# Kernel tuning notes

Hardware: AMD Instinct MI355X
Metric: run time of the kernel (lower is better)

The kernel has to match this reference:

```python
import jax, jax.numpy as jnp
import numpy as np

G, N, F_IN, H, C = 128, 512, 128, 128, 10
LAMB = 1.0
NEG_SLOPE = 0.2
P_EDGE = 32.0 / N  # avg degree ~32


def setup_inputs() -> dict:
    key = jax.random.key(0)
    ks = jax.random.split(key, 12)
    x = jax.random.normal(ks[0], (G, N, F_IN), dtype=jnp.float32)
    # symmetric 0/1 adjacency without self loops (per-graph dense block)
    a = (jax.random.uniform(ks[1], (G, N, N)) < P_EDGE).astype(jnp.float32)
    adj = jnp.maximum(a, jnp.swapaxes(a, 1, 2)) * (1.0 - jnp.eye(N, dtype=jnp.float32))

    def lin(k, fi, fo):
        return (jax.random.normal(k, (fi, fo), dtype=jnp.float32) / np.float32(np.sqrt(fi)))

    return {
        "x": x, "adj": adj,
        "W1": lin(ks[2], F_IN, H), "b1": jnp.zeros((H,), jnp.float32),
        "W2": lin(ks[3], H, H), "b2": jnp.zeros((H,), jnp.float32),
        "W3": lin(ks[4], H, H), "b3": jnp.zeros((H,), jnp.float32),
        "att1_s": 0.1 * jax.random.normal(ks[5], (H,), dtype=jnp.float32),
        "att1_d": 0.1 * jax.random.normal(ks[6], (H,), dtype=jnp.float32),
        "att2_s": 0.1 * jax.random.normal(ks[7], (H,), dtype=jnp.float32),
        "att2_d": 0.1 * jax.random.normal(ks[8], (H,), dtype=jnp.float32),
        "Wl1": lin(ks[9], 2 * H, H), "bl1": jnp.zeros((H,), jnp.float32),
        "Wl2": lin(ks[10], H, H // 2), "bl2": jnp.zeros((H // 2,), jnp.float32),
        "Wl3": lin(ks[11], H // 2, C), "bl3": jnp.zeros((C,), jnp.float32),
    }


def gcn(x, adj, W, b):
    # GCNConv: D^{-1/2} (A + I) D^{-1/2} X W + b  (self-loop weight 1, edge weights in adj)
    deg = adj.sum(-1) + 1.0                              # [G, n]
    dinv = jax.lax.rsqrt(deg)
    xw = x @ W                                           # [G, n, H]
    agg = jnp.einsum('gij,gjf->gif', adj, dinv[..., None] * xw)
    return dinv[..., None] * agg + (dinv * dinv)[..., None] * xw + b


def info_score(x, adj):
    # HGP-SL node information score: row-wise L1 norm of (I - D^{-1} A) X
    deg = jnp.maximum(adj.sum(-1), 1.0)
    agg = jnp.einsum('gij,gjf->gif', adj, x) / deg[..., None]
    return jnp.sum(jnp.abs(x - agg), axis=-1)            # [G, n]


def hgpsl_pool(x, adj, att_s, att_d, k):
    # top-k node selection by information score, then structure learning:
    # dense (sample=False) path: e_ij = leaky_relu(att.[x_i||x_j]) + lamb*A_ij, softmax over j
    s = info_score(x, adj)
    _, idx = jax.lax.top_k(s, k)                         # [G, k]
    xk = jnp.take_along_axis(x, idx[..., None], axis=1)  # [G, k, H]
    g = jnp.arange(x.shape[0])[:, None, None]
    ak = adj[g, idx[:, :, None], idx[:, None, :]]        # induced adjacency [G, k, k]
    e = jax.nn.leaky_relu((xk @ att_s)[:, :, None] + (xk @ att_d)[:, None, :], NEG_SLOPE)
    attn = jax.nn.softmax(e + LAMB * ak, axis=-1)        # new learned edge weights
    return xk, attn


def readout(x):
    # gmp || gap over nodes
    return jnp.concatenate([x.max(axis=1), x.mean(axis=1)], axis=-1)


def reference(x, adj, W1, b1, W2, b2, W3, b3, att1_s, att1_d, att2_s, att2_d,
              Wl1, bl1, Wl2, bl2, Wl3, bl3):
    h = jax.nn.relu(gcn(x, adj, W1, b1))
    h, a1 = hgpsl_pool(h, adj, att1_s, att1_d, N // 2)
    x1 = readout(h)
    h = jax.nn.relu(gcn(h, a1, W2, b2))
    h, a2 = hgpsl_pool(h, a1, att2_s, att2_d, N // 4)
    x2 = readout(h)
    h = jax.nn.relu(gcn(h, a2, W3, b3))
    x3 = readout(h)
    z = jax.nn.relu(x1) + jax.nn.relu(x2) + jax.nn.relu(x3)
    z = jax.nn.relu(z @ Wl1 + bl1)
    z = jax.nn.relu(z @ Wl2 + bl2)
    return jax.nn.softmax(z @ Wl3 + bl3, axis=-1)
```

## Files before the change

### kernel.cpp

```cpp
#include <hip/hip_runtime.h>

#define Gg   128
#define N1   512
#define FH   128
#define K1   256
#define K2   128

typedef unsigned short ush;
typedef __bf16 bf16x8 __attribute__((ext_vector_type(8)));
typedef float  floatx4 __attribute__((ext_vector_type(4)));

__device__ inline float wredsum(float v) {
#pragma unroll
    for (int o = 32; o; o >>= 1) v += __shfl_xor(v, o, 64);
    return v;
}
__device__ inline float wredmax(float v) {
#pragma unroll
    for (int o = 32; o; o >>= 1) v = fmaxf(v, __shfl_xor(v, o, 64));
    return v;
}
__device__ inline ush bf_rne(float x) {
    unsigned u = __float_as_uint(x);
    return (ush)((u + 0x7fffu + ((u >> 16) & 1u)) >> 16);
}
__device__ inline float bf2f(ush u) { return __uint_as_float((unsigned)u << 16); }
__device__ inline void split3(float v, ush& h, ush& m, ush& l) {
    h = bf_rne(v);
    float r1 = v - bf2f(h);
    m = bf_rne(r1);
    l = bf_rne(r1 - bf2f(m));
}

__global__ __launch_bounds__(256) void k_prep(const float* __restrict__ adj,
        float* __restrict__ dinv_gcn, float* __restrict__ dinv_info,
        unsigned* __restrict__ adjbits) {
    int wave = threadIdx.x >> 6, lane = threadIdx.x & 63;
    long long row = (long long)blockIdx.x * 4 + wave;
    const float* ar = adj + row * N1;
    float s = 0.f;
    unsigned myw = 0;
#pragma unroll
    for (int c = 0; c < 8; ++c) {
        float v = ar[c * 64 + lane];
        s += v;
        unsigned long long mk = __ballot(v != 0.0f);
        unsigned lo = (unsigned)mk, hi = (unsigned)(mk >> 32);
        if ((lane >> 1) == c) myw = (lane & 1) ? hi : lo;
    }
    if (lane < 16) adjbits[row * 16 + lane] = myw;
    s = wredsum(s);
    if (lane == 0) {
        dinv_gcn[row]  = rsqrtf(s + 1.0f);
        dinv_info[row] = 1.0f / fmaxf(s, 1.0f);
    }
}

__global__ __launch_bounds__(256) void k_gemm_rw(const float* __restrict__ A,
        const float* __restrict__ W, float* __restrict__ C,
        const float* __restrict__ rs) {
    __shared__ float Al[64][68];
    __shared__ float Wl[64][132];
    long long row0 = (long long)blockIdx.x * 64;
    int tid = threadIdx.x, tr = tid >> 4, tc = tid & 15;
    float acc[4][8] = {};
    for (int ch = 0; ch < 2; ++ch) {
        for (int p = tid; p < 1024; p += 256) {
            int r = p >> 4, c4 = p & 15;
            *(float4*)&Al[r][c4 * 4] = *(const float4*)(A + (row0 + r) * 128 + ch * 64 + c4 * 4);
        }
        for (int p = tid; p < 2048; p += 256) {
            int r = p >> 5, c4 = p & 31;
            *(float4*)&Wl[r][c4 * 4] = *(const float4*)(W + (ch * 64 + r) * 128 + c4 * 4);
        }
        __syncthreads();
        for (int k = 0; k < 64; ++k) {
            float4 w0 = *(const float4*)&Wl[k][tc * 8];
            float4 w1 = *(const float4*)&Wl[k][tc * 8 + 4];
            float w[8] = {w0.x, w0.y, w0.z, w0.w, w1.x, w1.y, w1.z, w1.w};
#pragma unroll
            for (int i = 0; i < 4; ++i) {
                float a = Al[tr * 4 + i][k];
#pragma unroll
                for (int j = 0; j < 8; ++j) acc[i][j] = fmaf(a, w[j], acc[i][j]);
            }
        }
        __syncthreads();
    }
#pragma unroll
    for (int i = 0; i < 4; ++i) {
        long long r = row0 + tr * 4 + i;
        float sc = rs ? rs[r] : 1.0f;
        *(float4*)(C + r * 128 + tc * 8)     = make_float4(sc * acc[i][0], sc * acc[i][1], sc * acc[i][2], sc * acc[i][3]);
        *(float4*)(C + r * 128 + tc * 8 + 4) = make_float4(sc * acc[i][4], sc * acc[i][5], sc * acc[i][6], sc * acc[i][7]);
    }
}

__global__ __launch_bounds__(256) void k_tsplit(const float* __restrict__ feat,
        ush* __restrict__ Thi, ush* __restrict__ Tmid, ush* __restrict__ Tlo) {
    __shared__ float tile[64 * 65];
    int b = blockIdx.x;
    int g = b >> 4, rb = (b >> 1) & 7, cb = b & 1;
    int t = threadIdx.x;
    {
        int r0 = t >> 4, c4 = t & 15;
#pragma unroll
        for (int i = 0; i < 4; ++i) {
            int r = r0 + i * 16;
            float4 v = *(const float4*)(feat + ((long long)g * 512 + rb * 64 + r) * 128 + cb * 64 + c4 * 4);
            tile[r * 65 + c4 * 4 + 0] = v.x;
            tile[r * 65 + c4 * 4 + 1] = v.y;
            tile[r * 65 + c4 * 4 + 2] = v.z;
            tile[r * 65 + c4 * 4 + 3] = v.w;
        }
    }
    __syncthreads();
    int tf = t >> 2, chunk = t & 3;
    ush hbuf[16] __attribute__((aligned(16)));
    ush mbuf[16] __attribute__((aligned(16)));
    ush lbuf[16] __attribute__((aligned(16)));
#pragma unroll
    for (int i = 0; i < 16; ++i) {
        int m = chunk * 16 + i;
        split3(tile[m * 65 + tf], hbuf[i], mbuf[i], lbuf[i]);
    }
    long long obase = ((long long)g * 128 + cb * 64 + tf) * 512 + rb * 64 + chunk * 16;
    *(uint4*)(Thi + obase)      = *(const uint4*)&hbuf[0];
    *(uint4*)(Thi + obase + 8)  = *(const uint4*)&hbuf[8];
    *(uint4*)(Tmid + obase)     = *(const uint4*)&mbuf[0];
    *(uint4*)(Tmid + obase + 8) = *(const uint4*)&mbuf[8];
    *(uint4*)(Tlo + obase)      = *(const uint4*)&lbuf[0];
    *(uint4*)(Tlo + obase + 8)  = *(const uint4*)&lbuf[8];
}

template<int EPI>
__global__ __launch_bounds__(256) void k_aggb(const unsigned* __restrict__ adjbits,
        const ush* __restrict__ Bhi, const ush* __restrict__ Bmid, const ush* __restrict__ Blo,
        const float* __restrict__ dvec, const float* __restrict__ hx,
        const float* __restrict__ bias, float* __restrict__ outH, float* __restrict__ outS) {
    __shared__ unsigned bitsL[64 * 17];
    __shared__ float sred[2][64];
    int b = blockIdx.x;
    int g  = (b & 7) + ((b >> 6) << 3);
    int rb = (b >> 3) & 7;
    int tid = threadIdx.x;
    int w = tid >> 6, lane = tid & 63;
    int wm = w >> 1, wn = w & 1;
    int ln = lane & 15, quad = lane >> 4;
    {
        int r = tid >> 2, w4 = (tid & 3) * 4;
        uint4 v = *(const uint4*)(adjbits + ((long long)(g * 512 + rb * 64 + r)) * 16 + w4);
        bitsL[r * 17 + w4 + 0] = v.x; bitsL[r * 17 + w4 + 1] = v.y;
        bitsL[r * 17 + w4 + 2] = v.z; bitsL[r * 17 + w4 + 3] = v.w;
    }
    __syncthreads();
    floatx4 acc[2][4];
#pragma unroll
    for (int i = 0; i < 2; ++i)
#pragma unroll
        for (int j = 0; j < 4; ++j) { floatx4 z = {0.f, 0.f, 0.f, 0.f}; acc[i][j] = z; }

    const long long bb = (long long)g * 128 * 512;
    for (int kt = 0; kt < 16; ++kt) {
        int kk = kt * 32;
        bf16x8 af[2];
#pragma unroll
        for (int tm = 0; tm < 2; ++tm) {
            unsigned word = bitsL[(wm * 32 + tm * 16 + ln) * 17 + kt];
            unsigned byte = (word >> (quad * 8)) & 0xffu;
            unsigned au[4] __attribute__((aligned(16)));
            au[0] = ((byte >> 0) & 1 ? 0x3F80u : 0u) | ((byte >> 1) & 1 ? 0x3F800000u : 0u);
            au[1] = ((byte >> 2) & 1 ? 0x3F80u : 0u) | ((byte >> 3) & 1 ? 0x3F800000u : 0u);
            au[2] = ((byte >> 4) & 1 ? 0x3F80u : 0u) | ((byte >> 5) & 1 ? 0x3F800000u : 0u);
            au[3] = ((byte >> 6) & 1 ? 0x3F80u : 0u) | ((byte >> 7) & 1 ? 0x3F800000u : 0u);
            af[tm] = *(const bf16x8*)au;
        }
#pragma unroll
        for (int tn = 0; tn < 4; ++tn) {
            long long off = bb + (long long)(wn * 64 + tn * 16 + ln) * 512 + kk + quad * 8;
            bf16x8 bh = *(const bf16x8*)(Bhi + off);
            bf16x8 bm = *(const bf16x8*)(Bmid + off);
            bf16x8 bl = *(const bf16x8*)(Blo + off);
#pragma unroll
            for (int tm = 0; tm < 2; ++tm) {
                acc[tm][tn] = __builtin_amdgcn_mfma_f32_16x16x32_bf16(af[tm], bh, acc[tm][tn], 0, 0, 0);
                acc[tm][tn] = __builtin_amdgcn_mfma_f32_16x16x32_bf16(af[tm], bm, acc[tm][tn], 0, 0, 0);
                acc[tm][tn] = __builtin_amdgcn_mfma_f32_16x16x32_bf16(af[tm], bl, acc[tm][tn], 0, 0, 0);
            }
        }
    }
    long long rowbase = (long long)g * 512 + rb * 64;
    if (EPI == 0) {
#pragma unroll
        for (int tm = 0; tm < 2; ++tm)
#pragma unroll
        for (int r = 0; r < 4; ++r) {
            long long grow = rowbase + wm * 32 + tm * 16 + quad * 4 + r;
            float di = dvec[grow];
#pragma unroll
            for (int tn = 0; tn < 4; ++tn) {
                int nc = wn * 64 + tn * 16 + ln;
                outH[grow * 128 + nc] =
                    fmaxf(fmaf(di, acc[tm][tn][r] + hx[grow * 128 + nc], bias[nc]), 0.f);
            }
        }
    } else {
#pragma unroll
        for (int tm = 0; tm < 2; ++tm)
#pragma unroll
        for (int r = 0; r < 4; ++r) {
            int ml = wm * 32 + tm * 16 + quad * 4 + r;
            long long grow = rowbase + ml;
            float di = dvec[grow];
            float v = 0.f;
#pragma unroll
            for (int tn = 0; tn < 4; ++tn) {
                int nc = wn * 64 + tn * 16 + ln;
                v += fabsf(hx[grow * 128 + nc] - acc[tm][tn][r] * di);
            }
            v += __shfl_xor(v, 1); v += __shfl_xor(v, 2);
            v += __shfl_xor(v, 4); v += __shfl_xor(v, 8);
            if (ln == 0) sred[wn][ml] = v;
        }
        __syncthreads();
        if (tid < 64) outS[rowbase + tid] = sred[0][tid] + sred[1][tid];
    }
}

template<int NT, int KSEL>
__global__ __launch_bounds__(256) void k_topk(const float* __restrict__ s, int* __restrict__ idx) {
    __shared__ unsigned long long keys[NT];
    int g = blockIdx.x;
    const float* sg = s + g * NT;
    for (int t = threadIdx.x; t < NT; t += 256) {
        unsigned int b = __float_as_uint(sg[t]);
        unsigned int ord = (b & 0x80000000u) ? ~b : (b | 0x80000000u);
        keys[t] = ((unsigned long long)(~ord) << 32) | (unsigned int)t;
    }
    __syncthreads();
    for (int k = 2; k <= NT; k <<= 1) {
        for (int j = k >> 1; j > 0; j >>= 1) {
            for (int i = threadIdx.x; i < NT; i += 256) {
                int l = i ^ j;
                if (l > i) {
                    bool dir = ((i & k) == 0);
                    unsigned long long a = keys[i], b2 = keys[l];
                    bool sw = dir ? (a > b2) : (a < b2);
                    if (sw) { keys[i] = b2; keys[l] = a; }
                }
            }
            __syncthreads();
        }
    }
    for (int t = threadIdx.x; t < KSEL; t += 256)
        idx[g * KSEL + t] = (int)(keys[t] & 0xffffffffu);
}

template<int KK>
__global__ __launch_bounds__(256) void k_gather(const float* __restrict__ h, int srcN,
        const int* __restrict__ idx, const float* __restrict__ atts, const float* __restrict__ attd,
        float* __restrict__ xk, float* __restrict__ as_, float* __restrict__ ad_) {
    int wave = threadIdx.x >> 6, lane = threadIdx.x & 63;
    int r = blockIdx.x * 4 + wave;
    int g = r / KK;
    int j = idx[r];
    float2 v = *(const float2*)(h + ((long long)g * srcN + j) * 128 + lane * 2);
    *(float2*)(xk + (long long)r * 128 + lane * 2) = v;
    float2 sv = *(const float2*)(atts + lane * 2);
    float2 dv = *(const float2*)(attd + lane * 2);
    float ps = v.x * sv.x + v.y * sv.y;
    float pd = v.x * dv.x + v.y * dv.y;
    ps = wredsum(ps); pd = wredsum(pd);
    if (lane == 0) { as_[r] = ps; ad_[r] = pd; }
}

__global__ __launch_bounds__(256) void k_attn1b(const unsigned* __restrict__ adjbits,
        const int* __restrict__ idx, const float* __restrict__ as_, const float* __restrict__ ad_,
        float* __restrict__ a1, float* __restrict__ dgo, float* __restrict__ dio) {
    __shared__ int   idxL[K1];
    __shared__ float adL[K1];
    __shared__ unsigned bitsW[4][20];
    int g = blockIdx.x / (K1 / 4);
    int wave = threadIdx.x >> 6, lane = threadIdx.x & 63;
    int i = (blockIdx.x % (K1 / 4)) * 4 + wave;
    for (int t = threadIdx.x; t < K1; t += 256) { idxL[t] = idx[g * K1 + t]; adL[t] = ad_[g * K1 + t]; }
    __syncthreads();
    int ri = idxL[i];
    if (lane < 4) {
        uint4 v = *(const uint4*)(adjbits + ((long long)(g * 512 + ri)) * 16 + lane * 4);
        bitsW[wave][lane * 4 + 0] = v.x; bitsW[wave][lane * 4 + 1] = v.y;
        bitsW[wave][lane * 4 + 2] = v.z; bitsW[wave][lane * 4 + 3] = v.w;
    }
    __syncthreads();
    float asi = as_[g * K1 + i];
    float vals[4];
    float m = -1e30f;
#pragma unroll
    for (int e = 0; e < 4; ++e) {
        int j = e * 64 + lane;
        float x = asi + adL[j];
        x = (x >= 0.f) ? x : 0.2f * x;
        int jj = idxL[j];
        unsigned bit = (bitsW[wave][jj >> 5] >> (jj & 31)) & 1u;
        x += (float)bit;
        vals[e] = x; m = fmaxf(m, x);
    }
    m = wredmax(m);
    float S = 0.f;
#pragma unroll
    for (int e = 0; e < 4; ++e) { vals[e] = expf(vals[e] - m); S += vals[e]; }
    S = wredsum(S);
    float inv = 1.f / S, rs = 0.f;
    float* orow = a1 + ((long long)g * K1 + i) * K1;
#pragma unroll
    for (int e = 0; e < 4; ++e) { float p = vals[e] * inv; rs += p; orow[e * 64 + lane] = p; }
    rs = wredsum(rs);
    if (lane == 0) { dgo[g * K1 + i] = rsqrtf(rs + 1.f); dio[g * K1 + i] = 1.f / fmaxf(rs, 1.f); }
}

template<int KK, int SRCN>
__global__ __launch_bounds__(256) void k_attn(const float* __restrict__ adjSrc,
        const int* __restrict__ idx, const float* __restrict__ as_, const float* __restrict__ ad_,
        float* __restrict__ attn, float* __restrict__ dgo, float* __restrict__ dio) {
    constexpr int E = KK / 64;
    __shared__ int   idxL[KK];
    __shared__ float adL[KK];
    __shared__ float rowL[4][SRCN];
    int bpg = KK / 4;
    int g = blockIdx.x / bpg;
    int wave = threadIdx.x >> 6, lane = threadIdx.x & 63;
    int i = (blockIdx.x % bpg) * 4 + wave;
    for (int t = threadIdx.x; t < KK; t += 256) { idxL[t] = idx[g * KK + t]; adL[t] = ad_[g * KK + t]; }
    __syncthreads();
    int ri = idxL[i];
    const float* arow = adjSrc + ((long long)g * SRCN + ri) * SRCN;
    for (int c = lane; c < SRCN; c += 64) rowL[wave][c] = arow[c];
    float asi = as_[g * KK + i];
    float vals[E];
    float m = -1e30f;
#pragma unroll
    for (int e = 0; e < E; ++e) {
        int j = e * 64 + lane;
        float x = asi + adL[j];
        x = (x >= 0.f) ? x : 0.2f * x;
        x += rowL[wave][idxL[j]];
        vals[e] = x; m = fmaxf(m, x);
    }
    m = wredmax(m);
    float S = 0.f;
#pragma unroll
    for (int e = 0; e < E; ++e) { vals[e] = expf(vals[e] - m); S += vals[e]; }
    S = wredsum(S);
    float inv = 1.f / S, rs = 0.f;
    float* orow = attn + ((long long)g * KK + i) * KK;
#pragma unroll
    for (int e = 0; e < E; ++e) { float p = vals[e] * inv; rs += p; orow[e * 64 + lane] = p; }
    rs = wredsum(rs);
    if (lane == 0) { dgo[g * KK + i] = rsqrtf(rs + 1.f); dio[g * KK + i] = 1.f / fmaxf(rs, 1.f); }
}

template<int KK>
__global__ __launch_bounds__(128) void k_readout(const float* __restrict__ xk, float* __restrict__ xo) {
    int g = blockIdx.x, f = threadIdx.x;
    const float* p = xk + (long long)g * KK * 128 + f;
    float m = -1e30f, s = 0.f;
    for (int r = 0; r < KK; ++r) { float v = p[r * 128]; m = fmaxf(m, v); s += v; }
    xo[g * 256 + f] = m;
    xo[g * 256 + 128 + f] = s * (1.0f / KK);
}

template<int KK, bool SCALEY, int EPI>
__global__ __launch_bounds__(256) void k_agg(const float* __restrict__ A, const float* __restrict__ Y,
        const float* __restrict__ dg, const float* __restrict__ di_,
        const float* __restrict__ bias, const float* __restrict__ hx,
        float* __restrict__ outH, float* __restrict__ outS) {
    __shared__ float Al[64][68];
    __shared__ float Yl[64][132];
    __shared__ float red[64][17];
    constexpr int RB = KK / 64;
    int g = blockIdx.x / RB;
    int rb = blockIdx.x % RB;
    const float* Ag = A + (long long)g * KK * KK;
    const float* Yg = Y + (long long)g * KK * 128;
    int tid = threadIdx.x, tr = tid >> 4, tc = tid & 15;
    float acc[4][8] = {};
    for (int ch = 0; ch < KK / 64; ++ch) {
        for (int p = tid; p < 1024; p += 256) {
            int r = p >> 4, c4 = p & 15;
            *(float4*)&Al[r][c4 * 4] = *(const float4*)(Ag + (rb * 64 + r) * KK + ch * 64 + c4 * 4);
        }
        for (int p = tid; p < 2048; p += 256) {
            int r = p >> 5, c4 = p & 31;
            float4 v = *(const float4*)(Yg + (ch * 64 + r) * 128 + c4 * 4);
            if (SCALEY) { float sc = dg[g * KK + ch * 64 + r]; v.x *= sc; v.y *= sc; v.z *= sc; v.w *= sc; }
            *(float4*)&Yl[r][c4 * 4] = v;
        }
        __syncthreads();
        for (int k = 0; k < 64; ++k) {
            float4 w0 = *(const float4*)&Yl[k][tc * 8];
            float4 w1 = *(const float4*)&Yl[k][tc * 8 + 4];
            float w[8] = {w0.x, w0.y, w0.z, w0.w, w1.x, w1.y, w1.z, w1.w};
#pragma unroll
            for (int i = 0; i < 4; ++i) {
                float a = Al[tr * 4 + i][k];
#pragma unroll
                for (int j = 0; j < 8; ++j) acc[i][j] = fmaf(a, w[j], acc[i][j]);
            }
        }
        __syncthreads();
    }
    int i0 = rb * 64 + tr * 4;
    if (EPI == 0) {
#pragma unroll
        for (int i = 0; i < 4; ++i) {
            long long gi = (long long)g * KK + i0 + i;
            float d = dg[gi], dd = d * d;
            float4 x0 = *(const float4*)(hx + gi * 128 + tc * 8);
            float4 x1 = *(const float4*)(hx + gi * 128 + tc * 8 + 4);
            float4 b0 = *(const float4*)(bias + tc * 8);
            float4 b1 = *(const float4*)(bias + tc * 8 + 4);
            float4 o0, o1;
            o0.x = fmaxf(fmaf(d, acc[i][0], fmaf(dd, x0.x, b0.x)), 0.f);
            o0.y = fmaxf(fmaf(d, acc[i][1], fmaf(dd, x0.y, b0.y)), 0.f);
            o0.z = fmaxf(fmaf(d, acc[i][2], fmaf(dd, x0.z, b0.z)), 0.f);
            o0.w = fmaxf(fmaf(d, acc[i][3], fmaf(dd, x0.w, b0.w)), 0.f);
            o1.x = fmaxf(fmaf(d, acc[i][4], fmaf(dd, x1.x, b1.x)), 0.f);
            o1.y = fmaxf(fmaf(d, acc[i][5], fmaf(dd, x1.y, b1.y)), 0.f);
            o1.z = fmaxf(fmaf(d, acc[i][6], fmaf(dd, x1.z, b1.z)), 0.f);
            o1.w = fmaxf(fmaf(d, acc[i][7], fmaf(dd, x1.w, b1.w)), 0.f);
            *(float4*)(outH + gi * 128 + tc * 8)     = o0;
            *(float4*)(outH + gi * 128 + tc * 8 + 4) = o1;
        }
    } else {
#pragma unroll
        for (int i = 0; i < 4; ++i) {
            long long gi = (long long)g * KK + i0 + i;
            float d = di_[gi];
            float4 x0 = *(const float4*)(hx + gi * 128 + tc * 8);
            float4 x1 = *(const float4*)(hx + gi * 128 + tc * 8 + 4);
            float p = fabsf(x0.x - acc[i][0] * d) + fabsf(x0.y - acc[i][1] * d)
                    + fabsf(x0.z - acc[i][2] * d) + fabsf(x0.w - acc[i][3] * d)
                    + fabsf(x1.x - acc[i][4] * d) + fabsf(x1.y - acc[i][5] * d)
                    + fabsf(x1.z - acc[i][6] * d) + fabsf(x1.w - acc[i][7] * d);
            red[tr * 4 + i][tc] = p;
        }
        __syncthreads();
        if (tid < 64) {
            float s = 0.f;
#pragma unroll
            for (int t = 0; t < 16; ++t) s += red[tid][t];
            outS[(long long)g * KK + rb * 64 + tid] = s;
        }
    }
}

__global__ __launch_bounds__(128) void k_mlp(const float* __restrict__ x1, const float* __restrict__ x2,
        const float* __restrict__ x3,
        const float* __restrict__ Wl1, const float* __restrict__ bl1,
        const float* __restrict__ Wl2, const float* __restrict__ bl2,
        const float* __restrict__ Wl3, const float* __restrict__ bl3,
        float* __restrict__ out) {
    __shared__ float z[256], z1[128], z2[64], lg[10];
    int g = blockIdx.x, t = threadIdx.x;
    for (int k = t; k < 256; k += 128)
        z[k] = fmaxf(x1[g * 256 + k], 0.f) + fmaxf(x2[g * 256 + k], 0.f) + fmaxf(x3[g * 256 + k], 0.f);
    __syncthreads();
    {
        float acc = bl1[t];
        for (int k = 0; k < 256; ++k) acc = fmaf(z[k], Wl1[k * 128 + t], acc);
        z1[t] = fmaxf(acc, 0.f);
    }
    __syncthreads();
    if (t < 64) {
        float acc = bl2[t];
        for (int k = 0; k < 128; ++k) acc = fmaf(z1[k], Wl2[k * 64 + t], acc);
        z2[t] = fmaxf(acc, 0.f);
    }
    __syncthreads();
    if (t < 10) {
        float acc = bl3[t];
        for (int k = 0; k < 64; ++k) acc = fmaf(z2[k], Wl3[k * 10 + t], acc);
        lg[t] = acc;
    }
    __syncthreads();
    if (t == 0) {
        float m = -1e30f;
        for (int c = 0; c < 10; ++c) m = fmaxf(m, lg[c]);
        float S = 0.f;
        float e[10];
        for (int c = 0; c < 10; ++c) { e[c] = expf(lg[c] - m); S += e[c]; }
        float inv = 1.f / S;
        for (int c = 0; c < 10; ++c) out[g * 10 + c] = e[c] * inv;
    }
}

extern "C" void kernel_launch(void* const* d_in, const int* in_sizes, int n_in,
                              void* d_out, int out_size, void* d_ws, size_t ws_size,
                              hipStream_t stream) {
    const float* x     = (const float*)d_in[0];
    const float* adj   = (const float*)d_in[1];
    const float* W1    = (const float*)d_in[2];
    const float* b1    = (const float*)d_in[3];
    const float* W2    = (const float*)d_in[4];
    const float* b2    = (const float*)d_in[5];
    const float* W3    = (const float*)d_in[6];
    const float* b3    = (const float*)d_in[7];
    const float* att1s = (const float*)d_in[8];
    const float* att1d = (const float*)d_in[9];
    const float* att2s = (const float*)d_in[10];
    const float* att2d = (const float*)d_in[11];
    const float* Wl1   = (const float*)d_in[12];
    const float* bl1   = (const float*)d_in[13];
    const float* Wl2   = (const float*)d_in[14];
    const float* bl2   = (const float*)d_in[15];
    const float* Wl3   = (const float*)d_in[16];
    const float* bl3   = (const float*)d_in[17];
    float* out = (float*)d_out;

    char* ws = (char*)d_ws;
    unsigned* adjbits = (unsigned*)(ws + 0);
    ush*   T1hi   = (ush*)  (ws + 8388608);
    ush*   T1mid  = (ush*)  (ws + 25165824);
    ush*   T1lo   = (ush*)  (ws + 41943040);
    ush*   T2hi   = (ush*)  (ws + 58720256);
    ush*   T2mid  = (ush*)  (ws + 75497472);
    ush*   T2lo   = (ush*)  (ws + 92274688);
    float* dxw1   = (float*)(ws + 109051904);
    float* h1     = dxw1;
    float* a1     = (float*)(ws + 142606336);
    float* xk1    = (float*)(ws + 176160768);
    float* xw2    = (float*)(ws + 192937984);
    float* h2     = (float*)(ws + 209715200);
    float* xk2    = (float*)(ws + 226492416);
    float* a2     = (float*)(ws + 234881024);
    float* xw3    = (float*)(ws + 243269632);
    float* h3     = (float*)(ws + 251658240);
    float* s1     = (float*)(ws + 260046848);
    int*   idx1   = (int*)  (ws + 260308992);
    float* as1    = (float*)(ws + 260571136);
    float* ad1    = (float*)(ws + 260702208);
    float* dinv_g1= (float*)(ws + 260833280);
    float* dinv_i1= (float*)(ws + 261095424);
    float* dinv_g2= (float*)(ws + 261357568);
    float* dinv_i2= (float*)(ws + 261488640);
    float* x1r    = (float*)(ws + 261619712);
    float* s2     = (float*)(ws + 261750784);
    int*   idx2   = (int*)  (ws + 261881856);
    float* as2    = (float*)(ws + 261947392);
    float* ad2    = (float*)(ws + 262012928);
    float* dinv_g3= (float*)(ws + 262078464);
    float* dinv_i3= (float*)(ws + 262144000);
    float* x2r    = (float*)(ws + 262209536);
    float* x3r    = (float*)(ws + 262340608);

    k_prep<<<Gg * N1 / 4, 256, 0, stream>>>(adj, dinv_g1, dinv_i1, adjbits);
    k_gemm_rw<<<Gg * N1 / 64, 256, 0, stream>>>(x, W1, dxw1, dinv_g1);
    k_tsplit<<<Gg * 16, 256, 0, stream>>>(dxw1, T1hi, T1mid, T1lo);
    k_aggb<0><<<Gg * 8, 256, 0, stream>>>(adjbits, T1hi, T1mid, T1lo, dinv_g1, dxw1, b1, h1, nullptr);
    k_tsplit<<<Gg * 16, 256, 0, stream>>>(h1, T2hi, T2mid, T2lo);
    k_aggb<1><<<Gg * 8, 256, 0, stream>>>(adjbits, T2hi, T2mid, T2lo, dinv_i1, h1, nullptr, nullptr, s1);
    k_topk<N1, K1><<<Gg, 256, 0, stream>>>(s1, idx1);
    k_gather<K1><<<Gg * K1 / 4, 256, 0, stream>>>(h1, N1, idx1, att1s, att1d, xk1, as1, ad1);
    k_readout<K1><<<Gg, 128, 0, stream>>>(xk1, x1r);
    k_attn1b<<<Gg * K1 / 4, 256, 0, stream>>>(adjbits, idx1, as1, ad1, a1, dinv_g2, dinv_i2);

    k_gemm_rw<<<Gg * K1 / 64, 256, 0, stream>>>(xk1, W2, xw2, nullptr);
    k_agg<K1, true, 0><<<Gg * (K1 / 64), 256, 0, stream>>>(a1, xw2, dinv_g2, dinv_i2, b2, xw2, h2, nullptr);
    k_agg<K1, false, 1><<<Gg * (K1 / 64), 256, 0, stream>>>(a1, h2, dinv_g2, dinv_i2, b2, h2, nullptr, s2);
    k_topk<K1, K2><<<Gg, 256, 0, stream>>>(s2, idx2);
    k_gather<K2><<<Gg * K2 / 4, 256, 0, stream>>>(h2, K1, idx2, att2s, att2d, xk2, as2, ad2);
    k_readout<K2><<<Gg, 128, 0, stream>>>(xk2, x2r);
    k_attn<K2, K1><<<Gg * K2 / 4, 256, 0, stream>>>(a1, idx2, as2, ad2, a2, dinv_g3, dinv_i3);

    k_gemm_rw<<<Gg * K2 / 64, 256, 0, stream>>>(xk2, W3, xw3, nullptr);
    k_agg<K2, true, 0><<<Gg * (K2 / 64), 256, 0, stream>>>(a2, xw3, dinv_g3, dinv_i3, b3, xw3, h3, nullptr);
    k_readout<K2><<<Gg, 128, 0, stream>>>(h3, x3r);

    k_mlp<<<Gg, 128, 0, stream>>>(x1r, x2r, x3r, Wl1, bl1, Wl2, bl2, Wl3, bl3, out);
}
```

Baseline: 708.1 us.

## Run pooled-graph aggregations on MFMA with 3-way bf16 split and prefetched loads

Replaces the fp32 FMA shared-memory aggregation kernels for the second and third GCN layers with MFMA-based kernels. Attention matrices and features are split into hi/mid/lo bf16 parts so products keep near-fp32 accuracy (six MFMA terms per tile). The attention kernels now write the split bf16 arrays directly, and the dense fp32 second attention matrix is no longer written. Adds register double-buffering of the B-operand loads in the layer-1 bitmask aggregation. This costs extra split kernels, a larger workspace and more MFMA work per output.

```diff
diff --git a/kernel.cpp b/kernel.cpp
--- a/kernel.cpp
+++ b/kernel.cpp
@@ -30,6 +30,15 @@
     float r1 = v - bf2f(h);
     m = bf_rne(r1);
     l = bf_rne(r1 - bf2f(m));
+}
+__device__ __forceinline__ bf16x8 expand_bits(unsigned word, int quad) {
+    unsigned byte = (word >> (quad * 8)) & 0xffu;
+    unsigned au[4] __attribute__((aligned(16)));
+    au[0] = ((byte & 1u)   ? 0x3F80u : 0u) | ((byte & 2u)   ? 0x3F800000u : 0u);
+    au[1] = ((byte & 4u)   ? 0x3F80u : 0u) | ((byte & 8u)   ? 0x3F800000u : 0u);
+    au[2] = ((byte & 16u)  ? 0x3F80u : 0u) | ((byte & 32u)  ? 0x3F800000u : 0u);
+    au[3] = ((byte & 64u)  ? 0x3F80u : 0u) | ((byte & 128u) ? 0x3F800000u : 0u);
+    return *(const bf16x8*)au;
 }
 
 __global__ __launch_bounds__(256) void k_prep(const float* __restrict__ adj,
@@ -96,18 +105,22 @@
     }
 }
 
+template<int KD>
 __global__ __launch_bounds__(256) void k_tsplit(const float* __restrict__ feat,
         ush* __restrict__ Thi, ush* __restrict__ Tmid, ush* __restrict__ Tlo) {
     __shared__ float tile[64 * 65];
     int b = blockIdx.x;
-    int g = b >> 4, rb = (b >> 1) & 7, cb = b & 1;
+    int cb = b & 1;
+    long long row0 = (long long)(b >> 1) * 64;
+    int g = (int)(row0 / KD);
+    int rk0 = (int)(row0 % KD);
     int t = threadIdx.x;
     {
         int r0 = t >> 4, c4 = t & 15;
 #pragma unroll
         for (int i = 0; i < 4; ++i) {
             int r = r0 + i * 16;
-            float4 v = *(const float4*)(feat + ((long long)g * 512 + rb * 64 + r) * 128 + cb * 64 + c4 * 4);
+            float4 v = *(const float4*)(feat + (row0 + r) * 128 + cb * 64 + c4 * 4);
             tile[r * 65 + c4 * 4 + 0] = v.x;
             tile[r * 65 + c4 * 4 + 1] = v.y;
             tile[r * 65 + c4 * 4 + 2] = v.z;
@@ -124,13 +137,64 @@
         int m = chunk * 16 + i;
         split3(tile[m * 65 + tf], hbuf[i], mbuf[i], lbuf[i]);
     }
-    long long obase = ((long long)g * 128 + cb * 64 + tf) * 512 + rb * 64 + chunk * 16;
+    long long obase = ((long long)g * 128 + cb * 64 + tf) * KD + rk0 + chunk * 16;
     *(uint4*)(Thi + obase)      = *(const uint4*)&hbuf[0];
     *(uint4*)(Thi + obase + 8)  = *(const uint4*)&hbuf[8];
     *(uint4*)(Tmid + obase)     = *(const uint4*)&mbuf[0];
     *(uint4*)(Tmid + obase + 8) = *(const uint4*)&mbuf[8];
     *(uint4*)(Tlo + obase)      = *(const uint4*)&lbuf[0];
     *(uint4*)(Tlo + obase + 8)  = *(const uint4*)&lbuf[8];
+}
+
+__device__ __forceinline__ void loadB4(const ush* __restrict__ Bhi, const ush* __restrict__ Bmid,
+        const ush* __restrict__ Blo, const long long* boff, int kk,
+        bf16x8* h, bf16x8* m, bf16x8* l) {
+#pragma unroll
+    for (int tn = 0; tn < 4; ++tn) {
+        h[tn] = *(const bf16x8*)(Bhi  + boff[tn] + kk);
+        m[tn] = *(const bf16x8*)(Bmid + boff[tn] + kk);
+        l[tn] = *(const bf16x8*)(Blo  + boff[tn] + kk);
+    }
+}
+__device__ __forceinline__ void loadA2(const ush* __restrict__ Ahi, const ush* __restrict__ Amid,
+        const ush* __restrict__ Alo, const long long* aoff, int kk,
+        bf16x8* h, bf16x8* m, bf16x8* l) {
+#pragma unroll
+    for (int tm = 0; tm < 2; ++tm) {
+        h[tm] = *(const bf16x8*)(Ahi  + aoff[tm] + kk);
+        m[tm] = *(const bf16x8*)(Amid + aoff[tm] + kk);
+        l[tm] = *(const bf16x8*)(Alo  + aoff[tm] + kk);
+    }
+}
+__device__ __forceinline__ void aggb_step(const unsigned* bitsL, int a0r, int a1r, int kt, int quad,
+        const bf16x8* Bh, const bf16x8* Bm, const bf16x8* Bl, floatx4 acc[2][4]) {
+    bf16x8 af0 = expand_bits(bitsL[a0r + kt], quad);
+    bf16x8 af1 = expand_bits(bitsL[a1r + kt], quad);
+#pragma unroll
+    for (int tn = 0; tn < 4; ++tn) {
+        acc[0][tn] = __builtin_amdgcn_mfma_f32_16x16x32_bf16(af0, Bh[tn], acc[0][tn], 0, 0, 0);
+        acc[1][tn] = __builtin_amdgcn_mfma_f32_16x16x32_bf16(af1, Bh[tn], acc[1][tn], 0, 0, 0);
+        acc[0][tn] = __builtin_amdgcn_mfma_f32_16x16x32_bf16(af0, Bm[tn], acc[0][tn], 0, 0, 0);
+        acc[1][tn] = __builtin_amdgcn_mfma_f32_16x16x32_bf16(af1, Bm[tn], acc[1][tn], 0, 0, 0);
+        acc[0][tn] = __builtin_amdgcn_mfma_f32_16x16x32_bf16(af0, Bl[tn], acc[0][tn], 0, 0, 0);
+        acc[1][tn] = __builtin_amdgcn_mfma_f32_16x16x32_bf16(af1, Bl[tn], acc[1][tn], 0, 0, 0);
+    }
+}
+__device__ __forceinline__ void aggs_step(const bf16x8* Ah, const bf16x8* Am, const bf16x8* Al,
+        const bf16x8* Bh, const bf16x8* Bm, const bf16x8* Bl, floatx4 acc[2][4]) {
+#pragma unroll
+    for (int tm = 0; tm < 2; ++tm)
+#pragma unroll
+    for (int tn = 0; tn < 4; ++tn) {
+        floatx4 a = acc[tm][tn];
+        a = __builtin_amdgcn_mfma_f32_16x16x32_bf16(Ah[tm], Bh[tn], a, 0, 0, 0);
+        a = __builtin_amdgcn_mfma_f32_16x16x32_bf16(Ah[tm], Bm[tn], a, 0, 0, 0);
+        a = __builtin_amdgcn_mfma_f32_16x16x32_bf16(Am[tm], Bh[tn], a, 0, 0, 0);
+        a = __builtin_amdgcn_mfma_f32_16x16x32_bf16(Ah[tm], Bl[tn], a, 0, 0, 0);
+        a = __builtin_amdgcn_mfma_f32_16x16x32_bf16(Al[tm], Bh[tn], a, 0, 0, 0);
+        a = __builtin_amdgcn_mfma_f32_16x16x32_bf16(Am[tm], Bm[tn], a, 0, 0, 0);
+        acc[tm][tn] = a;
+    }
 }
 
 template<int EPI>
@@ -161,35 +225,104 @@
         for (int j = 0; j < 4; ++j) { floatx4 z = {0.f, 0.f, 0.f, 0.f}; acc[i][j] = z; }
 
     const long long bb = (long long)g * 128 * 512;
-    for (int kt = 0; kt < 16; ++kt) {
-        int kk = kt * 32;
-        bf16x8 af[2];
-#pragma unroll
-        for (int tm = 0; tm < 2; ++tm) {
-            unsigned word = bitsL[(wm * 32 + tm * 16 + ln) * 17 + kt];
-            unsigned byte = (word >> (quad * 8)) & 0xffu;
-            unsigned au[4] __attribute__((aligned(16)));
-            au[0] = ((byte >> 0) & 1 ? 0x3F80u : 0u) | ((byte >> 1) & 1 ? 0x3F800000u : 0u);
-            au[1] = ((byte >> 2) & 1 ? 0x3F80u : 0u) | ((byte >> 3) & 1 ? 0x3F800000u : 0u);
-            au[2] = ((byte >> 4) & 1 ? 0x3F80u : 0u) | ((byte >> 5) & 1 ? 0x3F800000u : 0u);
-            au[3] = ((byte >> 6) & 1 ? 0x3F80u : 0u) | ((byte >> 7) & 1 ? 0x3F800000u : 0u);
-            af[tm] = *(const bf16x8*)au;
-        }
-#pragma unroll
-        for (int tn = 0; tn < 4; ++tn) {
-            long long off = bb + (long long)(wn * 64 + tn * 16 + ln) * 512 + kk + quad * 8;
-            bf16x8 bh = *(const bf16x8*)(Bhi + off);
-            bf16x8 bm = *(const bf16x8*)(Bmid + off);
-            bf16x8 bl = *(const bf16x8*)(Blo + off);
-#pragma unroll
-            for (int tm = 0; tm < 2; ++tm) {
-                acc[tm][tn] = __builtin_amdgcn_mfma_f32_16x16x32_bf16(af[tm], bh, acc[tm][tn], 0, 0, 0);
-                acc[tm][tn] = __builtin_amdgcn_mfma_f32_16x16x32_bf16(af[tm], bm, acc[tm][tn], 0, 0, 0);
-                acc[tm][tn] = __builtin_amdgcn_mfma_f32_16x16x32_bf16(af[tm], bl, acc[tm][tn], 0, 0, 0);
+    long long boff[4];
+#pragma unroll
+    for (int tn = 0; tn < 4; ++tn)
+        boff[tn] = bb + (long long)(wn * 64 + tn * 16 + ln) * 512 + quad * 8;
+    int a0r = (wm * 32 + ln) * 17;
+    int a1r = (wm * 32 + 16 + ln) * 17;
+
+    bf16x8 Xh[4], Xm[4], Xl[4], Yh[4], Ym[4], Yl[4];
+    loadB4(Bhi, Bmid, Blo, boff, 0, Xh, Xm, Xl);
+    for (int kt = 0; kt < 16; kt += 2) {
+        loadB4(Bhi, Bmid, Blo, boff, (kt + 1) * 32, Yh, Ym, Yl);
+        aggb_step(bitsL, a0r, a1r, kt, quad, Xh, Xm, Xl, acc);
+        if (kt + 2 < 16) loadB4(Bhi, Bmid, Blo, boff, (kt + 2) * 32, Xh, Xm, Xl);
+        aggb_step(bitsL, a0r, a1r, kt + 1, quad, Yh, Ym, Yl, acc);
+    }
+    long long rowbase = (long long)g * 512 + rb * 64;
+    if (EPI == 0) {
+#pragma unroll
+        for (int tm = 0; tm < 2; ++tm)
+#pragma unroll
+        for (int r = 0; r < 4; ++r) {
+            long long grow = rowbase + wm * 32 + tm * 16 + quad * 4 + r;
+            float di = dvec[grow];
+#pragma unroll
+            for (int tn = 0; tn < 4; ++tn) {
+                int nc = wn * 64 + tn * 16 + ln;
+                outH[grow * 128 + nc] =
+                    fmaxf(fmaf(di, acc[tm][tn][r] + hx[grow * 128 + nc], bias[nc]), 0.f);
             }
         }
-    }
-    long long rowbase = (long long)g * 512 + rb * 64;
+    } else {
+#pragma unroll
+        for (int tm = 0; tm < 2; ++tm)
+#pragma unroll
+        for (int r = 0; r < 4; ++r) {
+            int ml = wm * 32 + tm * 16 + quad * 4 + r;
+            long long grow = rowbase + ml;
+            float di = dvec[grow];
+            float v = 0.f;
+#pragma unroll
+            for (int tn = 0; tn < 4; ++tn) {
+                int nc = wn * 64 + tn * 16 + ln;
+                v += fabsf(hx[grow * 128 + nc] - acc[tm][tn][r] * di);
+            }
+            v += __shfl_xor(v, 1); v += __shfl_xor(v, 2);
+            v += __shfl_xor(v, 4); v += __shfl_xor(v, 8);
+            if (ln == 0) sred[wn][ml] = v;
+        }
+        __syncthreads();
+        if (tid < 64) outS[rowbase + tid] = sred[0][tid] + sred[1][tid];
+    }
+}
+
+template<int KD, int EPI>
+__global__ __launch_bounds__(256) void k_aggs(
+        const ush* __restrict__ Ahi, const ush* __restrict__ Amid, const ush* __restrict__ Alo,
+        const ush* __restrict__ Yhi, const ush* __restrict__ Ymid, const ush* __restrict__ Ylo,
+        const float* __restrict__ dvec, const float* __restrict__ hx,
+        const float* __restrict__ bias, float* __restrict__ outH, float* __restrict__ outS) {
+    __shared__ float sred[2][64];
+    constexpr int BPG = KD / 64;
+    constexpr int KT = KD / 32;
+    int b = blockIdx.x;
+    int g  = (b & 7) + ((b / (8 * BPG)) << 3);
+    int rb = (b >> 3) & (BPG - 1);
+    int tid = threadIdx.x;
+    int w = tid >> 6, lane = tid & 63;
+    int wm = w >> 1, wn = w & 1;
+    int ln = lane & 15, quad = lane >> 4;
+    floatx4 acc[2][4];
+#pragma unroll
+    for (int i = 0; i < 2; ++i)
+#pragma unroll
+        for (int j = 0; j < 4; ++j) { floatx4 z = {0.f, 0.f, 0.f, 0.f}; acc[i][j] = z; }
+
+    long long aoff[2], boff[4];
+#pragma unroll
+    for (int tm = 0; tm < 2; ++tm)
+        aoff[tm] = ((long long)g * KD + rb * 64 + wm * 32 + tm * 16 + ln) * KD + quad * 8;
+#pragma unroll
+    for (int tn = 0; tn < 4; ++tn)
+        boff[tn] = ((long long)g * 128 + wn * 64 + tn * 16 + ln) * KD + quad * 8;
+
+    bf16x8 XAh[2], XAm[2], XAl[2], YAh[2], YAm[2], YAl[2];
+    bf16x8 XBh[4], XBm[4], XBl[4], YBh[4], YBm[4], YBl[4];
+    loadA2(Ahi, Amid, Alo, aoff, 0, XAh, XAm, XAl);
+    loadB4(Yhi, Ymid, Ylo, boff, 0, XBh, XBm, XBl);
+    for (int kt = 0; kt < KT; kt += 2) {
+        loadA2(Ahi, Amid, Alo, aoff, (kt + 1) * 32, YAh, YAm, YAl);
+        loadB4(Yhi, Ymid, Ylo, boff, (kt + 1) * 32, YBh, YBm, YBl);
+        aggs_step(XAh, XAm, XAl, XBh, XBm, XBl, acc);
+        if (kt + 2 < KT) {
+            loadA2(Ahi, Amid, Alo, aoff, (kt + 2) * 32, XAh, XAm, XAl);
+            loadB4(Yhi, Ymid, Ylo, boff, (kt + 2) * 32, XBh, XBm, XBl);
+        }
+        aggs_step(YAh, YAm, YAl, YBh, YBm, YBl, acc);
+    }
+    long long rowbase = (long long)g * KD + rb * 64;
     if (EPI == 0) {
 #pragma unroll
         for (int tm = 0; tm < 2; ++tm)
@@ -276,10 +409,12 @@
 
 __global__ __launch_bounds__(256) void k_attn1b(const unsigned* __restrict__ adjbits,
         const int* __restrict__ idx, const float* __restrict__ as_, const float* __restrict__ ad_,
-        float* __restrict__ a1, float* __restrict__ dgo, float* __restrict__ dio) {
+        float* __restrict__ a1, ush* __restrict__ Ahi, ush* __restrict__ Amid, ush* __restrict__ Alo,
+        float* __restrict__ dgo, float* __restrict__ dio) {
     __shared__ int   idxL[K1];
     __shared__ float adL[K1];
     __shared__ unsigned bitsW[4][20];
+    __shared__ float rowL[4][K1];
     int g = blockIdx.x / (K1 / 4);
     int wave = threadIdx.x >> 6, lane = threadIdx.x & 63;
     int i = (blockIdx.x % (K1 / 4)) * 4 + wave;
@@ -313,33 +448,42 @@
     float inv = 1.f / S, rs = 0.f;
     float* orow = a1 + ((long long)g * K1 + i) * K1;
 #pragma unroll
-    for (int e = 0; e < 4; ++e) { float p = vals[e] * inv; rs += p; orow[e * 64 + lane] = p; }
+    for (int e = 0; e < 4; ++e) {
+        float p = vals[e] * inv; rs += p;
+        orow[e * 64 + lane] = p;
+        rowL[wave][e * 64 + lane] = p;
+    }
     rs = wredsum(rs);
     if (lane == 0) { dgo[g * K1 + i] = rsqrtf(rs + 1.f); dio[g * K1 + i] = 1.f / fmaxf(rs, 1.f); }
-}
-
-template<int KK, int SRCN>
-__global__ __launch_bounds__(256) void k_attn(const float* __restrict__ adjSrc,
+    long long sb = ((long long)g * K1 + i) * K1 + lane * 4;
+    ush hb[4], mb[4], lb[4];
+#pragma unroll
+    for (int q = 0; q < 4; ++q) split3(rowL[wave][lane * 4 + q], hb[q], mb[q], lb[q]);
+    *(ushort4*)(Ahi  + sb) = make_ushort4(hb[0], hb[1], hb[2], hb[3]);
+    *(ushort4*)(Amid + sb) = make_ushort4(mb[0], mb[1], mb[2], mb[3]);
+    *(ushort4*)(Alo  + sb) = make_ushort4(lb[0], lb[1], lb[2], lb[3]);
+}
+
+__global__ __launch_bounds__(256) void k_attn2(const float* __restrict__ a1,
         const int* __restrict__ idx, const float* __restrict__ as_, const float* __restrict__ ad_,
-        float* __restrict__ attn, float* __restrict__ dgo, float* __restrict__ dio) {
-    constexpr int E = KK / 64;
-    __shared__ int   idxL[KK];
-    __shared__ float adL[KK];
-    __shared__ float rowL[4][SRCN];
-    int bpg = KK / 4;
-    int g = blockIdx.x / bpg;
+        ush* __restrict__ Ahi, ush* __restrict__ Amid, ush* __restrict__ Alo,
+        float* __restrict__ dgo) {
+    __shared__ int   idxL[K2];
+    __shared__ float adL[K2];
+    __shared__ float rowL[4][K1];
+    int g = blockIdx.x / (K2 / 4);
     int wave = threadIdx.x >> 6, lane = threadIdx.x & 63;
-    int i = (blockIdx.x % bpg) * 4 + wave;
-    for (int t = threadIdx.x; t < KK; t += 256) { idxL[t] = idx[g * KK + t]; adL[t] = ad_[g * KK + t]; }
+    int i = (blockIdx.x % (K2 / 4)) * 4 + wave;
+    for (int t = threadIdx.x; t < K2; t += 256) { idxL[t] = idx[g * K2 + t]; adL[t] = ad_[g * K2 + t]; }
     __syncthreads();
     int ri = idxL[i];
-    const float* arow = adjSrc + ((long long)g * SRCN + ri) * SRCN;
-    for (int c = lane; c < SRCN; c += 64) rowL[wave][c] = arow[c];
-    float asi = as_[g * KK + i];
-    float vals[E];
+    const float* arow = a1 + ((long long)g * K1 + ri) * K1;
+    for (int c = lane; c < K1; c += 64) rowL[wave][c] = arow[c];
+    float asi = as_[g * K2 + i];
+    float vals[2];
     float m = -1e30f;
 #pragma unroll
-    for (int e = 0; e < E; ++e) {
+    for (int e = 0; e < 2; ++e) {
         int j = e * 64 + lane;
         float x = asi + adL[j];
         x = (x >= 0.f) ? x : 0.2f * x;
@@ -349,14 +493,23 @@
     m = wredmax(m);
     float S = 0.f;
 #pragma unroll
-    for (int e = 0; e < E; ++e) { vals[e] = expf(vals[e] - m); S += vals[e]; }
+    for (int e = 0; e < 2; ++e) { vals[e] = expf(vals[e] - m); S += vals[e]; }
     S = wredsum(S);
     float inv = 1.f / S, rs = 0.f;
-    float* orow = attn + ((long long)g * KK + i) * KK;
-#pragma unroll
-    for (int e = 0; e < E; ++e) { float p = vals[e] * inv; rs += p; orow[e * 64 + lane] = p; }
+#pragma unroll
+    for (int e = 0; e < 2; ++e) {
+        float p = vals[e] * inv; rs += p;
+        rowL[wave][e * 64 + lane] = p;
+    }
     rs = wredsum(rs);
-    if (lane == 0) { dgo[g * KK + i] = rsqrtf(rs + 1.f); dio[g * KK + i] = 1.f / fmaxf(rs, 1.f); }
+    if (lane == 0) dgo[g * K2 + i] = rsqrtf(rs + 1.f);
+    long long sb = ((long long)g * K2 + i) * K2 + lane * 2;
+    ush hb[2], mb[2], lb[2];
+#pragma unroll
+    for (int q = 0; q < 2; ++q) split3(rowL[wave][lane * 2 + q], hb[q], mb[q], lb[q]);
+    *(ushort2*)(Ahi  + sb) = make_ushort2(hb[0], hb[1]);
+    *(ushort2*)(Amid + sb) = make_ushort2(mb[0], mb[1]);
+    *(ushort2*)(Alo  + sb) = make_ushort2(lb[0], lb[1]);
 }
 
 template<int KK>
@@ -367,91 +520,6 @@
     for (int r = 0; r < KK; ++r) { float v = p[r * 128]; m = fmaxf(m, v); s += v; }
     xo[g * 256 + f] = m;
     xo[g * 256 + 128 + f] = s * (1.0f / KK);
-}
-
-template<int KK, bool SCALEY, int EPI>
-__global__ __launch_bounds__(256) void k_agg(const float* __restrict__ A, const float* __restrict__ Y,
-        const float* __restrict__ dg, const float* __restrict__ di_,
-        const float* __restrict__ bias, const float* __restrict__ hx,
-        float* __restrict__ outH, float* __restrict__ outS) {
-    __shared__ float Al[64][68];
-    __shared__ float Yl[64][132];
-    __shared__ float red[64][17];
-    constexpr int RB = KK / 64;
-    int g = blockIdx.x / RB;
-    int rb = blockIdx.x % RB;
-    const float* Ag = A + (long long)g * KK * KK;
-    const float* Yg = Y + (long long)g * KK * 128;
-    int tid = threadIdx.x, tr = tid >> 4, tc = tid & 15;
-    float acc[4][8] = {};
-    for (int ch = 0; ch < KK / 64; ++ch) {
-        for (int p = tid; p < 1024; p += 256) {
-            int r = p >> 4, c4 = p & 15;
-            *(float4*)&Al[r][c4 * 4] = *(const float4*)(Ag + (rb * 64 + r) * KK + ch * 64 + c4 * 4);
-        }
-        for (int p = tid; p < 2048; p += 256) {
-            int r = p >> 5, c4 = p & 31;
-            float4 v = *(const float4*)(Yg + (ch * 64 + r) * 128 + c4 * 4);
-            if (SCALEY) { float sc = dg[g * KK + ch * 64 + r]; v.x *= sc; v.y *= sc; v.z *= sc; v.w *= sc; }
-            *(float4*)&Yl[r][c4 * 4] = v;
-        }
-        __syncthreads();
-        for (int k = 0; k < 64; ++k) {
-            float4 w0 = *(const float4*)&Yl[k][tc * 8];
-            float4 w1 = *(const float4*)&Yl[k][tc * 8 + 4];
-            float w[8] = {w0.x, w0.y, w0.z, w0.w, w1.x, w1.y, w1.z, w1.w};
-#pragma unroll
-            for (int i = 0; i < 4; ++i) {
-                float a = Al[tr * 4 + i][k];
-#pragma unroll
-                for (int j = 0; j < 8; ++j) acc[i][j] = fmaf(a, w[j], acc[i][j]);
-            }
-        }
-        __syncthreads();
-    }
-    int i0 = rb * 64 + tr * 4;
-    if (EPI == 0) {
-#pragma unroll
-        for (int i = 0; i < 4; ++i) {
-            long long gi = (long long)g * KK + i0 + i;
-            float d = dg[gi], dd = d * d;
-            float4 x0 = *(const float4*)(hx + gi * 128 + tc * 8);
-            float4 x1 = *(const float4*)(hx + gi * 128 + tc * 8 + 4);
-            float4 b0 = *(const float4*)(bias + tc * 8);
-            float4 b1 = *(const float4*)(bias + tc * 8 + 4);
-            float4 o0, o1;
-            o0.x = fmaxf(fmaf(d, acc[i][0], fmaf(dd, x0.x, b0.x)), 0.f);
-            o0.y = fmaxf(fmaf(d, acc[i][1], fmaf(dd, x0.y, b0.y)), 0.f);
-            o0.z = fmaxf(fmaf(d, acc[i][2], fmaf(dd, x0.z, b0.z)), 0.f);
-            o0.w = fmaxf(fmaf(d, acc[i][3], fmaf(dd, x0.w, b0.w)), 0.f);
-            o1.x = fmaxf(fmaf(d, acc[i][4], fmaf(dd, x1.x, b1.x)), 0.f);
-            o1.y = fmaxf(fmaf(d, acc[i][5], fmaf(dd, x1.y, b1.y)), 0.f);
-            o1.z = fmaxf(fmaf(d, acc[i][6], fmaf(dd, x1.z, b1.z)), 0.f);
-            o1.w = fmaxf(fmaf(d, acc[i][7], fmaf(dd, x1.w, b1.w)), 0.f);
-            *(float4*)(outH + gi * 128 + tc * 8)     = o0;
-            *(float4*)(outH + gi * 128 + tc * 8 + 4) = o1;
-        }
-    } else {
-#pragma unroll
-        for (int i = 0; i < 4; ++i) {
-            long long gi = (long long)g * KK + i0 + i;
-            float d = di_[gi];
-            float4 x0 = *(const float4*)(hx + gi * 128 + tc * 8);
-            float4 x1 = *(const float4*)(hx + gi * 128 + tc * 8 + 4);
-            float p = fabsf(x0.x - acc[i][0] * d) + fabsf(x0.y - acc[i][1] * d)
-                    + fabsf(x0.z - acc[i][2] * d) + fabsf(x0.w - acc[i][3] * d)
-                    + fabsf(x1.x - acc[i][4] * d) + fabsf(x1.y - acc[i][5] * d)
-                    + fabsf(x1.z - acc[i][6] * d) + fabsf(x1.w - acc[i][7] * d);
-            red[tr * 4 + i][tc] = p;
-        }
-        __syncthreads();
-        if (tid < 64) {
-            float s = 0.f;
-#pragma unroll
-            for (int t = 0; t < 16; ++t) s += red[tid][t];
-            outS[(long long)g * KK + rb * 64 + tid] = s;
-        }
-    }
 }
 
 __global__ __launch_bounds__(128) void k_mlp(const float* __restrict__ x1, const float* __restrict__ x2,
@@ -519,61 +587,81 @@
 
     char* ws = (char*)d_ws;
     unsigned* adjbits = (unsigned*)(ws + 0);
-    ush*   T1hi   = (ush*)  (ws + 8388608);
-    ush*   T1mid  = (ush*)  (ws + 25165824);
-    ush*   T1lo   = (ush*)  (ws + 41943040);
-    ush*   T2hi   = (ush*)  (ws + 58720256);
-    ush*   T2mid  = (ush*)  (ws + 75497472);
-    ush*   T2lo   = (ush*)  (ws + 92274688);
-    float* dxw1   = (float*)(ws + 109051904);
+    ush*   T1hi   = (ush*)  (ws + 4194304);
+    ush*   T1mid  = (ush*)  (ws + 20971520);
+    ush*   T1lo   = (ush*)  (ws + 37748736);
+    ush*   T2hi   = (ush*)  (ws + 54525952);
+    ush*   T2mid  = (ush*)  (ws + 71303168);
+    ush*   T2lo   = (ush*)  (ws + 88080384);
+    float* dxw1   = (float*)(ws + 104857600);
     float* h1     = dxw1;
-    float* a1     = (float*)(ws + 142606336);
-    float* xk1    = (float*)(ws + 176160768);
-    float* xw2    = (float*)(ws + 192937984);
-    float* h2     = (float*)(ws + 209715200);
-    float* xk2    = (float*)(ws + 226492416);
-    float* a2     = (float*)(ws + 234881024);
-    float* xw3    = (float*)(ws + 243269632);
-    float* h3     = (float*)(ws + 251658240);
-    float* s1     = (float*)(ws + 260046848);
-    int*   idx1   = (int*)  (ws + 260308992);
-    float* as1    = (float*)(ws + 260571136);
-    float* ad1    = (float*)(ws + 260702208);
-    float* dinv_g1= (float*)(ws + 260833280);
-    float* dinv_i1= (float*)(ws + 261095424);
-    float* dinv_g2= (float*)(ws + 261357568);
-    float* dinv_i2= (float*)(ws + 261488640);
-    float* x1r    = (float*)(ws + 261619712);
-    float* s2     = (float*)(ws + 261750784);
-    int*   idx2   = (int*)  (ws + 261881856);
-    float* as2    = (float*)(ws + 261947392);
-    float* ad2    = (float*)(ws + 262012928);
-    float* dinv_g3= (float*)(ws + 262078464);
-    float* dinv_i3= (float*)(ws + 262144000);
-    float* x2r    = (float*)(ws + 262209536);
-    float* x3r    = (float*)(ws + 262340608);
+    float* a1     = (float*)(ws + 138412032);
+    ush*   A1hi   = (ush*)  (ws + 171966464);
+    ush*   A1mid  = (ush*)  (ws + 188743680);
+    ush*   A1lo   = (ush*)  (ws + 205520896);
+    float* xk1    = (float*)(ws + 222298112);
+    float* dxw2   = (float*)(ws + 239075328);
+    ush*   Y2hi   = (ush*)  (ws + 255852544);
+    ush*   Y2mid  = (ush*)  (ws + 264241152);
+    ush*   Y2lo   = (ush*)  (ws + 272629760);
+    float* h2     = (float*)(ws + 281018368);
+    ush*   H2hi   = (ush*)  (ws + 297795584);
+    ush*   H2mid  = (ush*)  (ws + 306184192);
+    ush*   H2lo   = (ush*)  (ws + 314572800);
+    float* xk2    = (float*)(ws + 322961408);
+    ush*   A2hi   = (ush*)  (ws + 331350016);
+    ush*   A2mid  = (ush*)  (ws + 335544320);
+    ush*   A2lo   = (ush*)  (ws + 339738624);
+    float* dxw3   = (float*)(ws + 343932928);
+    ush*   Y3hi   = (ush*)  (ws + 352321536);
+    ush*   Y3mid  = (ush*)  (ws + 356515840);
+    ush*   Y3lo   = (ush*)  (ws + 360710144);
+    float* h3     = (float*)(ws + 364904448);
+    float* s1     = (float*)(ws + 373293056);
+    int*   idx1   = (int*)  (ws + 373555200);
+    float* as1    = (float*)(ws + 373817344);
+    float* ad1    = (float*)(ws + 373948416);
+    float* dinv_g1= (float*)(ws + 374079488);
+    float* dinv_i1= (float*)(ws + 374341632);
+    float* dinv_g2= (float*)(ws + 374603776);
+    float* dinv_i2= (float*)(ws + 374734848);
+    float* x1r    = (float*)(ws + 374865920);
+    float* s2     = (float*)(ws + 374996992);
+    int*   idx2   = (int*)  (ws + 375128064);
+    float* as2    = (float*)(ws + 375193600);
+    float* ad2    = (float*)(ws + 375259136);
+    float* dinv_g3= (float*)(ws + 375324672);
+    float* x2r    = (float*)(ws + 375390208);
+    float* x3r    = (float*)(ws + 375521280);
 
     k_prep<<<Gg * N1 / 4, 256, 0, stream>>>(adj, dinv_g1, dinv_i1, adjbits);
     k_gemm_rw<<<Gg * N1 / 64, 256, 0, stream>>>(x, W1, dxw1, dinv_g1);
-    k_tsplit<<<Gg * 16, 256, 0, stream>>>(dxw1, T1hi, T1mid, T1lo);
+    k_tsplit<N1><<<Gg * 16, 256, 0, stream>>>(dxw1, T1hi, T1mid, T1lo);
     k_aggb<0><<<Gg * 8, 256, 0, stream>>>(adjbits, T1hi, T1mid, T1lo, dinv_g1, dxw1, b1, h1, nullptr);
-    k_tsplit<<<Gg * 16, 256, 0, stream>>>(h1, T2hi, T2mid, T2lo);
+    k_tsplit<N1><<<Gg * 16, 256, 0, stream>>>(h1, T2hi, T2mid, T2lo);
     k_aggb<1><<<Gg * 8, 256, 0, stream>>>(adjbits, T2hi, T2mid, T2lo, dinv_i1, h1, nullptr, nullptr, s1);
     k_topk<N1, K1><<<Gg, 256, 0, stream>>>(s1, idx1);
     k_gather<K1><<<Gg * K1 / 4, 256, 0, stream>>>(h1, N1, idx1, att1s, att1d, xk1, as1, ad1);
     k_readout<K1><<<Gg, 128, 0, stream>>>(xk1, x1r);
-    k_attn1b<<<Gg * K1 / 4, 256, 0, stream>>>(adjbits, idx1, as1, ad1, a1, dinv_g2, dinv_i2);
-
-    k_gemm_rw<<<Gg * K1 / 64, 256, 0, stream>>>(xk1, W2, xw2, nullptr);
-    k_agg<K1, true, 0><<<Gg * (K1 / 64), 256, 0, stream>>>(a1, xw2, dinv_g2, dinv_i2, b2, xw2, h2, nullptr);
-    k_agg<K1, false, 1><<<Gg * (K1 / 64), 256, 0, stream>>>(a1, h2, dinv_g2, dinv_i2, b2, h2, nullptr, s2);
+    k_attn1b<<<Gg * K1 / 4, 256, 0, stream>>>(adjbits, idx1, as1, ad1, a1, A1hi, A1mid, A1lo,
+                                              dinv_g2, dinv_i2);
+
+    k_gemm_rw<<<Gg * K1 / 64, 256, 0, stream>>>(xk1, W2, dxw2, dinv_g2);
+    k_tsplit<K1><<<Gg * 8, 256, 0, stream>>>(dxw2, Y2hi, Y2mid, Y2lo);
+    k_aggs<K1, 0><<<Gg * 4, 256, 0, stream>>>(A1hi, A1mid, A1lo, Y2hi, Y2mid, Y2lo,
+                                              dinv_g2, dxw2, b2, h2, nullptr);
+    k_tsplit<K1><<<Gg * 8, 256, 0, stream>>>(h2, H2hi, H2mid, H2lo);
+    k_aggs<K1, 1><<<Gg * 4, 256, 0, stream>>>(A1hi, A1mid, A1lo, H2hi, H2mid, H2lo,
+                                              dinv_i2, h2, nullptr, nullptr, s2);
     k_topk<K1, K2><<<Gg, 256, 0, stream>>>(s2, idx2);
     k_gather<K2><<<Gg * K2 / 4, 256, 0, stream>>>(h2, K1, idx2, att2s, att2d, xk2, as2, ad2);
     k_readout<K2><<<Gg, 128, 0, stream>>>(xk2, x2r);
-    k_attn<K2, K1><<<Gg * K2 / 4, 256, 0, stream>>>(a1, idx2, as2, ad2, a2, dinv_g3, dinv_i3);
-
-    k_gemm_rw<<<Gg * K2 / 64, 256, 0, stream>>>(xk2, W3, xw3, nullptr);
-    k_agg<K2, true, 0><<<Gg * (K2 / 64), 256, 0, stream>>>(a2, xw3, dinv_g3, dinv_i3, b3, xw3, h3, nullptr);
+    k_attn2<<<Gg * K2 / 4, 256, 0, stream>>>(a1, idx2, as2, ad2, A2hi, A2mid, A2lo, dinv_g3);
+
+    k_gemm_rw<<<Gg * K2 / 64, 256, 0, stream>>>(xk2, W3, dxw3, dinv_g3);
+    k_tsplit<K2><<<Gg * 4, 256, 0, stream>>>(dxw3, Y3hi, Y3mid, Y3lo);
+    k_aggs<K2, 0><<<Gg * 2, 256, 0, stream>>>(A2hi, A2mid, A2lo, Y3hi, Y3mid, Y3lo,
+                                              dinv_g3, dxw3, b3, h3, nullptr);
     k_readout<K2><<<Gg, 128, 0, stream>>>(h3, x3r);
 
     k_mlp<<<Gg, 128, 0, stream>>>(x1r, x2r, x3r, Wl1, bl1, Wl2, bl2, Wl3, bl3, out);
```

Result: slower. 736.5 us (+4.0%).
